# Kernel tuning notes

Hardware: AMD Instinct MI355X
Metric: run time of the kernel (lower is better)

Reference implementation:

```python
import jax, jax.numpy as jnp
import numpy as np

N = 100000
E = 3200000
NEG_SLOPE = 0.2


def _gat(x, W, a_src, a_dst, b, src, dst, n):
    """PyG-style GATConv (eval mode, self-loops already appended to src/dst)."""
    H, C = a_src.shape
    h = (x @ W).reshape(n, H, C)                       # [N,H,C]
    es = jnp.einsum('nhc,hc->nh', h, a_src)            # per-node src logits
    ed = jnp.einsum('nhc,hc->nh', h, a_dst)
    e = jax.nn.leaky_relu(es[src] + ed[dst], NEG_SLOPE)  # [E,H]
    m = jax.ops.segment_max(e, dst, num_segments=n)    # stable softmax per dst
    ee = jnp.exp(e - m[dst])
    z = jax.ops.segment_sum(ee, dst, num_segments=n)
    alpha = ee / z[dst]                                # softmax over in-edges
    out = jax.ops.segment_sum(h[src] * alpha[:, :, None], dst, num_segments=n)
    return out.reshape(n, H * C) + b


def setup_inputs() -> dict:
    key = jax.random.key(0)
    ks = jax.random.split(key, 25)
    rn = lambda k, s, sc=0.1: jax.random.normal(k, s, dtype=jnp.float32) * sc
    return {
        'x1': rn(ks[0], (N, 8), 1.0),
        'x2': rn(ks[1], (N, 10), 1.0),
        'edge_index': jax.random.randint(ks[2], (2, E), 0, N, dtype=jnp.int32),
        'num_nodes': N,
        'Wq': rn(ks[3], (8, 16)), 'bq': rn(ks[4], (16,)),
        'Wk': rn(ks[5], (10, 16)), 'bk': rn(ks[6], (16,)),
        'Wv': rn(ks[7], (18, 16)), 'bv': rn(ks[8], (16,)),
        'W1': rn(ks[9], (16, 32)), 'a1s': rn(ks[10], (8, 4)), 'a1d': rn(ks[11], (8, 4)), 'b1': rn(ks[12], (32,)),
        'W2': rn(ks[13], (32, 16)), 'a2s': rn(ks[14], (4, 4)), 'a2d': rn(ks[15], (4, 4)), 'b2': rn(ks[16], (16,)),
        'W3': rn(ks[17], (16, 8)), 'a3s': rn(ks[18], (2, 4)), 'a3d': rn(ks[19], (2, 4)), 'b3': rn(ks[20], (8,)),
        'Wl2': rn(ks[21], (8, 1)),
    }


def reference(x1, x2, edge_index, num_nodes, Wq, bq, Wk, bk, Wv, bv,
              W1, a1s, a1d, b1, W2, a2s, a2d, b2, W3, a3s, a3d, b3, Wl2):
    n = num_nodes
    q = x1 @ Wq + bq                                   # [N,16]
    k = x2 @ Wk + bk                                   # [N,16]
    v = jnp.concatenate([x1, x2], axis=1) @ Wv + bv    # [N,16]
    score = jnp.sum(q * k, axis=1)                     # bmm(q[:,None,:], k[:,:,None]).squeeze()
    attw = jax.nn.softmax(score)[:, None]              # softmax over all nodes
    fused = attw * v                                   # [N,16]

    sl = jnp.arange(n, dtype=edge_index.dtype)         # GATConv adds self-loops
    src = jnp.concatenate([edge_index[0], sl])
    dst = jnp.concatenate([edge_index[1], sl])

    h1 = _gat(fused, W1, a1s, a1d, b1, src, dst, n)    # [N,32]
    h2 = _gat(h1, W2, a2s, a2d, b2, src, dst, n)       # [N,16]
    x4 = _gat(h2, W3, a3s, a3d, b3, src, dst, n)       # [N,8]; dropout=identity (eval)

    # Row-normalized adjacency (no self loops), expressed as O(E) segment ops.
    r, c = edge_index[0], edge_index[1]
    deg = jax.ops.segment_sum(jnp.ones_like(r, dtype=x4.dtype), r, num_segments=n)
    inv = jnp.where(deg > 0, 1.0 / deg, 0.0)[:, None]
    R3 = jax.ops.segment_sum(x4[c], r, num_segments=n) * inv  # Adj_norm @ x4
    local = jnp.sum(x4 * R3, axis=1, keepdims=True)    # sum_j Adjn[i,j]*(x4_i . x4_j)
    glob = R3 @ Wl2                                    # lin2 (no bias)
    return local + glob                                # [N,1]
```

## Files before the change

kernel.cpp:

```cpp
#include <hip/hip_runtime.h>

#define TPB 256
#define CAP 9216
#define EPB 4096
#define OFSW 784
#define GBPAD 784

typedef float f32x4 __attribute__((ext_vector_type(4)));
typedef float f32x2 __attribute__((ext_vector_type(2)));
typedef unsigned u32x4 __attribute__((ext_vector_type(4)));

__device__ __forceinline__ float lrelu(float x) { return x > 0.f ? x : 0.2f * x; }

__device__ __forceinline__ unsigned bfr(float x) {
  unsigned u = __float_as_uint(x);
  return (u + 0x7FFFu + ((u >> 16) & 1u)) >> 16;
}
__device__ __forceinline__ unsigned pk(float a, float b) { return bfr(a) | (bfr(b) << 16); }
__device__ __forceinline__ float ubf(unsigned us) { return __uint_as_float(us << 16); }

__global__ void __launch_bounds__(TPB) k_bucket(
    const int* __restrict__ ei, int E, int N,
    unsigned* __restrict__ items2, int* __restrict__ ofs)
{
  __shared__ int hist[1024];
  __shared__ int lofs[1024];
  __shared__ int scan_s[TPB];
  __shared__ unsigned stage[2 * EPB];
  int tid = threadIdx.x;
  for (int i = tid; i < 1024; i += TPB) hist[i] = 0;
  int s0 = blockIdx.x * EPB;
  int nE = min(EPB, E - s0);
  int sv[16], dv[16];
  __syncthreads();
#pragma unroll
  for (int k = 0; k < 4; k++) {
    int li = tid * 4 + k * TPB * 4;
    if (li + 3 < nE) {
      int4 s4 = *(const int4*)(ei + s0 + li);
      int4 d4 = *(const int4*)(ei + E + s0 + li);
      sv[k*4+0] = s4.x; sv[k*4+1] = s4.y; sv[k*4+2] = s4.z; sv[k*4+3] = s4.w;
      dv[k*4+0] = d4.x; dv[k*4+1] = d4.y; dv[k*4+2] = d4.z; dv[k*4+3] = d4.w;
#pragma unroll
      for (int j = 0; j < 4; j++) {
        atomicAdd(&hist[dv[k*4+j] >> 8], 1);
        atomicAdd(&hist[(N + sv[k*4+j]) >> 8], 1);
      }
    } else {
      for (int j = 0; j < 4; j++) {
        if (li + j < nE) {
          sv[k*4+j] = ei[s0 + li + j];
          dv[k*4+j] = ei[E + s0 + li + j];
          atomicAdd(&hist[dv[k*4+j] >> 8], 1);
          atomicAdd(&hist[(N + sv[k*4+j]) >> 8], 1);
        }
      }
    }
  }
  __syncthreads();
  int b0 = tid * 4;
  int c0 = hist[b0], c1 = hist[b0 + 1], c2 = hist[b0 + 2], c3 = hist[b0 + 3];
  int tsum = c0 + c1 + c2 + c3;
  scan_s[tid] = tsum;
  __syncthreads();
#pragma unroll
  for (int o = 1; o < TPB; o <<= 1) {
    int t = (tid >= o) ? scan_s[tid - o] : 0;
    __syncthreads();
    scan_s[tid] += t;
    __syncthreads();
  }
  int run = scan_s[tid] - tsum;
  int cs[4] = {c0, c1, c2, c3};
#pragma unroll
  for (int j = 0; j < 4; j++) {
    int b = b0 + j;
    lofs[b] = run;
    hist[b] = 0;
    run += cs[j];
  }
  __syncthreads();
#pragma unroll
  for (int k = 0; k < 16; k++) {
    int li = tid * 4 + (k >> 2) * TPB * 4 + (k & 3);
    if (li < nE) {
      int s = sv[k], d = dv[k];
      int b1 = d >> 8;
      int p1 = lofs[b1] + atomicAdd(&hist[b1], 1);
      stage[p1] = ((unsigned)(d & 255) << 24) | (unsigned)s;
      int k2 = N + s, b2 = k2 >> 8;
      int p2 = lofs[b2] + atomicAdd(&hist[b2], 1);
      stage[p2] = ((unsigned)(k2 & 255) << 24) | (unsigned)d;
    }
  }
  __syncthreads();
  int total = 2 * nE;
  size_t obase = (size_t)blockIdx.x * (2 * EPB);
  for (int idx = tid; idx < total; idx += TPB)
    __builtin_nontemporal_store(stage[idx], items2 + obase + idx);
  int orow = blockIdx.x * OFSW;
  for (int i = tid; i < OFSW; i += TPB)
    ofs[orow + i] = lofs[i];
}

__global__ void __launch_bounds__(TPB) k_t(
    const int* __restrict__ ofs, int* __restrict__ ofsT, int nB)
{
  __shared__ int tile[32][33];
  int lx = threadIdx.x & 31, ly = threadIdx.x >> 5;
  int b0 = blockIdx.y * 32, k0 = blockIdx.x * 32;
#pragma unroll
  for (int r = 0; r < 32; r += 8) {
    int b = b0 + ly + r, k = k0 + lx;
    tile[ly + r][lx] = (b < nB && k < OFSW) ? ofs[b * OFSW + k] : 0;
  }
  __syncthreads();
#pragma unroll
  for (int r = 0; r < 32; r += 8) {
    int k = k0 + ly + r, b = b0 + lx;
    if (k < OFSW && b < GBPAD) ofsT[k * GBPAD + b] = tile[lx][ly + r];
  }
}

__global__ void __launch_bounds__(TPB) k_csr2(
    const int* __restrict__ ofsT, const unsigned* __restrict__ items2, int nB,
    unsigned* __restrict__ items, int* __restrict__ rowptr, int* __restrict__ rowend, int n2)
{
  __shared__ unsigned stage[CAP];
  __shared__ int cnt_s[TPB], scan_s[TPB], off_s[TPB];
  int tid = threadIdx.x, k = blockIdx.x;
  cnt_s[tid] = 0;
  int o0[4], cl[4];
  int tsum = 0;
#pragma unroll
  for (int m = 0; m < 4; m++) {
    int b = tid + m * TPB;
    if (b < nB) {
      int a0 = ofsT[(size_t)k * GBPAD + b];
      int a1 = ofsT[(size_t)(k + 1) * GBPAD + b];
      o0[m] = a0; cl[m] = a1 - a0;
    } else { o0[m] = 0; cl[m] = 0; }
    tsum += cl[m];
  }
  scan_s[tid] = tsum;
  __syncthreads();
#pragma unroll
  for (int o = 1; o < TPB; o <<= 1) {
    int t = (tid >= o) ? scan_s[tid - o] : 0;
    __syncthreads();
    scan_s[tid] += t;
    __syncthreads();
  }
  int cnt = min(scan_s[TPB - 1], CAP);
  int dst = scan_s[tid] - tsum;
#pragma unroll
  for (int m = 0; m < 4; m++) {
    int b = tid + m * TPB;
    const unsigned* src = items2 + (size_t)b * (2 * EPB) + o0[m];
    int c = cl[m];
    int j = 0;
    int head = (4 - (o0[m] & 3)) & 3; if (head > c) head = c;
    for (; j < head; j++) { int p = dst + j; if (p < CAP) stage[p] = src[j]; }
    for (; j + 3 < c; j += 4) {
      u32x4 v = *(const u32x4*)(src + j);
      int p = dst + j;
      if (p + 3 < CAP) {
        stage[p] = v.x; stage[p+1] = v.y; stage[p+2] = v.z; stage[p+3] = v.w;
      } else {
        if (p < CAP) stage[p] = v.x;
        if (p+1 < CAP) stage[p+1] = v.y;
        if (p+2 < CAP) stage[p+2] = v.z;
        if (p+3 < CAP) stage[p+3] = v.w;
      }
    }
    for (; j < c; j++) { int p = dst + j; if (p < CAP) stage[p] = src[j]; }
    dst += c;
  }
  __syncthreads();
  for (int i = tid; i < cnt; i += TPB) atomicAdd(&cnt_s[stage[i] >> 24], 1);
  __syncthreads();
  int v = cnt_s[tid];
  scan_s[tid] = v;
  __syncthreads();
#pragma unroll
  for (int o = 1; o < TPB; o <<= 1) {
    int t = (tid >= o) ? scan_s[tid - o] : 0;
    __syncthreads();
    scan_s[tid] += t;
    __syncthreads();
  }
  int excl = scan_s[tid] - v;
  off_s[tid] = excl;
  size_t bbase = (size_t)k * CAP;
  int g = k * 256 + tid;
  if (g < n2) { rowptr[g] = (int)bbase + excl; rowend[g] = (int)bbase + excl + v; }
  cnt_s[tid] = 0;
  __syncthreads();
  for (int i = tid; i < cnt; i += TPB) {
    unsigned u = stage[i];
    int kk = u >> 24;
    int r = atomicAdd(&cnt_s[kk], 1);
    items[bbase + off_s[kk] + r] = u & 0xFFFFFFu;
  }
}


__global__ void __launch_bounds__(TPB) k_score(
    const float* __restrict__ x1, const float* __restrict__ x2,
    const float* __restrict__ Wq, const float* __restrict__ bq,
    const float* __restrict__ Wk, const float* __restrict__ bk,
    float* __restrict__ escore, float* __restrict__ sumexp, int N)
{
  __shared__ float sWq[128], sWk[160], sbq[16], sbk[16];
  for (int i = threadIdx.x; i < 128; i += TPB) sWq[i] = Wq[i];
  for (int i = threadIdx.x; i < 160; i += TPB) sWk[i] = Wk[i];
  if (threadIdx.x < 16) { sbq[threadIdx.x] = bq[threadIdx.x]; sbk[threadIdx.x] = bk[threadIdx.x]; }
  __syncthreads();
  int n = blockIdx.x * TPB + threadIdx.x;
  float e = 0.f;
  if (n < N) {
    float a[8], b[10];
#pragma unroll
    for (int i = 0; i < 8; i++) a[i] = x1[n*8 + i];
#pragma unroll
    for (int i = 0; i < 10; i++) b[i] = x2[n*10 + i];
    float score = 0.f;
#pragma unroll
    for (int j = 0; j < 16; j++) {
      float q = sbq[j], k = sbk[j];
#pragma unroll
      for (int i = 0; i < 8; i++) q += a[i] * sWq[i*16 + j];
#pragma unroll
      for (int i = 0; i < 10; i++) k += b[i] * sWk[i*16 + j];
      score += q * k;
    }
    e = __expf(score);
    escore[n] = e;
  }
  float v = e;
#pragma unroll
  for (int off = 32; off > 0; off >>= 1) v += __shfl_down(v, off);
  __shared__ float red[TPB / 64];
  if ((threadIdx.x & 63) == 0) red[threadIdx.x >> 6] = v;
  __syncthreads();
  if (threadIdx.x == 0) {
    float s = 0.f;
#pragma unroll
    for (int w = 0; w < TPB / 64; w++) s += red[w];
    atomicAdd(sumexp, s);
  }
}

__global__ void __launch_bounds__(TPB) k_A1(
    const float* __restrict__ x1, const float* __restrict__ x2,
    const float* __restrict__ Wv, const float* __restrict__ bv,
    const float* __restrict__ W1, const float* __restrict__ a1s, const float* __restrict__ a1d,
    const float* __restrict__ escore, const float* __restrict__ sumexp,
    unsigned* __restrict__ rec1a, unsigned* __restrict__ rec1b,
    float* __restrict__ ed, int N)
{
  __shared__ float sWv[288], sbv[16], sW1[512], sas[32], sad[32];
  for (int i = threadIdx.x; i < 288; i += TPB) sWv[i] = Wv[i];
  for (int i = threadIdx.x; i < 512; i += TPB) sW1[i] = W1[i];
  if (threadIdx.x < 16) sbv[threadIdx.x] = bv[threadIdx.x];
  if (threadIdx.x < 32) { sas[threadIdx.x] = a1s[threadIdx.x]; sad[threadIdx.x] = a1d[threadIdx.x]; }
  __syncthreads();
  int n = blockIdx.x * TPB + threadIdx.x;
  if (n >= N) return;
  float w = escore[n] / sumexp[0];
  float f[16];
  {
    float a[8], b[10];
#pragma unroll
    for (int i = 0; i < 8; i++) a[i] = x1[n*8 + i];
#pragma unroll
    for (int i = 0; i < 10; i++) b[i] = x2[n*10 + i];
#pragma unroll
    for (int j = 0; j < 16; j++) {
      float v = sbv[j];
#pragma unroll
      for (int i = 0; i < 8; i++) v += a[i] * sWv[i*16 + j];
#pragma unroll
      for (int i = 0; i < 10; i++) v += b[i] * sWv[(8 + i)*16 + j];
      f[j] = w * v;
    }
  }
  float hr[32], esv[8], edv[8];
#pragma unroll
  for (int j = 0; j < 32; j++) {
    float s = 0.f;
#pragma unroll
    for (int i = 0; i < 16; i++) s += f[i] * sW1[i*32 + j];
    hr[j] = s;
  }
#pragma unroll
  for (int hh = 0; hh < 8; hh++) {
    float s = 0.f, d = 0.f;
#pragma unroll
    for (int c = 0; c < 4; c++) { s += hr[hh*4+c]*sas[hh*4+c]; d += hr[hh*4+c]*sad[hh*4+c]; }
    esv[hh] = s; edv[hh] = d;
  }
  unsigned* ra = rec1a + (size_t)n*10;
  unsigned* rb = rec1b + (size_t)n*10;
  ra[0] = pk(esv[0], esv[1]); ra[1] = pk(esv[2], esv[3]);
  rb[0] = pk(esv[4], esv[5]); rb[1] = pk(esv[6], esv[7]);
#pragma unroll
  for (int hh = 0; hh < 4; hh++) {
    ra[2+2*hh] = pk(hr[hh*4+0], hr[hh*4+1]);
    ra[3+2*hh] = pk(hr[hh*4+2], hr[hh*4+3]);
    rb[2+2*hh] = pk(hr[16+hh*4+0], hr[16+hh*4+1]);
    rb[3+2*hh] = pk(hr[16+hh*4+2], hr[16+hh*4+3]);
  }
  f32x4 e0 = {edv[0], edv[1], edv[2], edv[3]};
  f32x4 e1 = {edv[4], edv[5], edv[6], edv[7]};
  *(f32x4*)(ed + n*8)     = e0;
  *(f32x4*)(ed + n*8 + 4) = e1;
}

__global__ void __launch_bounds__(TPB) k_B2(
    const float* __restrict__ W2, const float* __restrict__ a2s, const float* __restrict__ a2d,
    const float* __restrict__ X,
    unsigned* __restrict__ rec2, float* __restrict__ ed, int N)
{
  __shared__ float sW[512], sas[16], sad[16];
  for (int i = threadIdx.x; i < 512; i += TPB) sW[i] = W2[i];
  if (threadIdx.x < 16) { sas[threadIdx.x] = a2s[threadIdx.x]; sad[threadIdx.x] = a2d[threadIdx.x]; }
  __syncthreads();
  int n = blockIdx.x * TPB + threadIdx.x;
  if (n >= N) return;
  float Xr[32];
#pragma unroll
  for (int i = 0; i < 8; i++) {
    f32x4 t = __builtin_nontemporal_load((const f32x4*)(X + n*32) + i);
    Xr[i*4+0] = t.x; Xr[i*4+1] = t.y; Xr[i*4+2] = t.z; Xr[i*4+3] = t.w;
  }
  float hr[16];
#pragma unroll
  for (int j = 0; j < 16; j++) {
    float s = 0.f;
#pragma unroll
    for (int f = 0; f < 32; f++) s += Xr[f] * sW[f*16 + j];
    hr[j] = s;
  }
  float esv[4], edv[4];
#pragma unroll
  for (int hh = 0; hh < 4; hh++) {
    float s = 0.f, d = 0.f;
#pragma unroll
    for (int c = 0; c < 4; c++) { s += hr[hh*4+c]*sas[hh*4+c]; d += hr[hh*4+c]*sad[hh*4+c]; }
    esv[hh] = s; edv[hh] = d;
  }
  unsigned* r = rec2 + (size_t)n*10;
  r[0] = pk(esv[0], esv[1]); r[1] = pk(esv[2], esv[3]);
#pragma unroll
  for (int hh = 0; hh < 4; hh++) {
    r[2+2*hh] = pk(hr[hh*4+0], hr[hh*4+1]);
    r[3+2*hh] = pk(hr[hh*4+2], hr[hh*4+3]);
  }
  f32x4 e0 = {edv[0], edv[1], edv[2], edv[3]};
  *(f32x4*)(ed + n*8) = e0;
}

__global__ void __launch_bounds__(TPB) k_B3(
    const float* __restrict__ W3, const float* __restrict__ a3s, const float* __restrict__ a3d,
    const float* __restrict__ X3,
    unsigned* __restrict__ rec3, float* __restrict__ ed, int N)
{
  __shared__ float sW[128], sas[8], sad[8];
  for (int i = threadIdx.x; i < 128; i += TPB) sW[i] = W3[i];
  if (threadIdx.x < 8) { sas[threadIdx.x] = a3s[threadIdx.x]; sad[threadIdx.x] = a3d[threadIdx.x]; }
  __syncthreads();
  int n = blockIdx.x * TPB + threadIdx.x;
  if (n >= N) return;
  float Xr[16];
#pragma unroll
  for (int i = 0; i < 4; i++) {
    f32x4 t = __builtin_nontemporal_load((const f32x4*)(X3 + n*16) + i);
    Xr[i*4+0] = t.x; Xr[i*4+1] = t.y; Xr[i*4+2] = t.z; Xr[i*4+3] = t.w;
  }
  float hr[8];
#pragma unroll
  for (int j = 0; j < 8; j++) {
    float s = 0.f;
#pragma unroll
    for (int f = 0; f < 16; f++) s += Xr[f] * sW[f*8 + j];
    hr[j] = s;
  }
  unsigned* r = rec3 + (size_t)n*8;
#pragma unroll
  for (int hh = 0; hh < 2; hh++) {
    float s = 0.f, d = 0.f;
#pragma unroll
    for (int c = 0; c < 4; c++) { s += hr[hh*4+c]*sas[hh*4+c]; d += hr[hh*4+c]*sad[hh*4+c]; }
    u32x4 q = { __float_as_uint(s),
                pk(hr[hh*4+0], hr[hh*4+1]), pk(hr[hh*4+2], hr[hh*4+3]), 0u };
    __builtin_nontemporal_store(q, (u32x4*)(r + hh*4));
    ed[n*8 + hh] = d;
  }
}

template<int OS, int HOFF>
__global__ void __launch_bounds__(TPB) k_gat4(
    const int* __restrict__ rowptr, const int* __restrict__ rowend, const int* __restrict__ col,
    const unsigned* __restrict__ rec, const float* __restrict__ ed,
    const float* __restrict__ bias, float* __restrict__ out, int N)
{
  int wave = (blockIdx.x * TPB + threadIdx.x) >> 6;
  if (wave >= N) return;
  int lane = threadIdx.x & 63;
  int hh = lane & 3, j = lane >> 2;
  int d = wave;
  int e0 = rowptr[d], deg = rowend[d] - e0;
  float edv = ed[d*8 + HOFF + hh];
  float z = 0.f;
  f32x4 acc = {0.f, 0.f, 0.f, 0.f};
  for (int t = j; t <= deg; t += 16) {
    int s = (t == deg) ? d : __builtin_nontemporal_load(col + e0 + t);
    const unsigned* rp = rec + (size_t)s*10;
    unsigned ew = rp[hh >> 1];
    uint2 hv = *(const uint2*)(rp + 2 + 2*hh);
    float esv = ubf((ew >> ((hh & 1) * 16)) & 0xFFFFu);
    float w = __expf(lrelu(esv + edv));
    z += w;
    acc.x += w * ubf(hv.x & 0xFFFFu); acc.y += w * ubf(hv.x >> 16);
    acc.z += w * ubf(hv.y & 0xFFFFu); acc.w += w * ubf(hv.y >> 16);
  }
#pragma unroll
  for (int m = 4; m < 64; m <<= 1) {
    z += __shfl_xor(z, m);
    acc.x += __shfl_xor(acc.x, m); acc.y += __shfl_xor(acc.y, m);
    acc.z += __shfl_xor(acc.z, m); acc.w += __shfl_xor(acc.w, m);
  }
  if (j == 0) {
    float inv = 1.f / z;
    const f32x4 bb = *(const f32x4*)(bias + (HOFF + hh)*4);
    f32x4 o = { acc.x*inv + bb.x, acc.y*inv + bb.y, acc.z*inv + bb.z, acc.w*inv + bb.w };
    __builtin_nontemporal_store(o, (f32x4*)(out + (size_t)d*OS + (HOFF + hh)*4));
  }
}

__global__ void __launch_bounds__(TPB) k_gat3(
    const int* __restrict__ rowptr, const int* __restrict__ rowend, const int* __restrict__ col,
    const unsigned* __restrict__ rec, const float* __restrict__ ed,
    const float* __restrict__ b3, float* __restrict__ x4, int N)
{
  int wave = (blockIdx.x * TPB + threadIdx.x) >> 6;
  if (wave >= N) return;
  int lane = threadIdx.x & 63;
  int hh = lane & 1, j = lane >> 1;
  int d = wave;
  int e0 = rowptr[d], deg = rowend[d] - e0;
  float edv = ed[d*8 + hh];
  float z = 0.f;
  f32x4 acc = {0.f, 0.f, 0.f, 0.f};
  for (int t = j; t <= deg; t += 32) {
    int s = (t == deg) ? d : __builtin_nontemporal_load(col + e0 + t);
    u32x4 q = *(const u32x4*)(rec + (size_t)s*8 + hh*4);
    float w = __expf(lrelu(__uint_as_float(q.x) + edv));
    z += w;
    acc.x += w * ubf(q.y & 0xFFFFu); acc.y += w * ubf(q.y >> 16);
    acc.z += w * ubf(q.z & 0xFFFFu); acc.w += w * ubf(q.z >> 16);
  }
#pragma unroll
  for (int m = 2; m < 64; m <<= 1) {
    z += __shfl_xor(z, m);
    acc.x += __shfl_xor(acc.x, m); acc.y += __shfl_xor(acc.y, m);
    acc.z += __shfl_xor(acc.z, m); acc.w += __shfl_xor(acc.w, m);
  }
  if (j == 0) {
    float inv = 1.f / z;
    const f32x4 bb = *(const f32x4*)(b3 + hh*4);
    f32x4 o = { acc.x*inv + bb.x, acc.y*inv + bb.y, acc.z*inv + bb.z, acc.w*inv + bb.w };
    __builtin_nontemporal_store(o, (f32x4*)(x4 + d*8 + hh*4));
  }
}

__global__ void __launch_bounds__(TPB) k_adj_final(
    const int* __restrict__ rowptr, const int* __restrict__ rowend, const int* __restrict__ col,
    const float* __restrict__ x4, const float* __restrict__ Wl2,
    float* __restrict__ out, int N)
{
  __shared__ float sW[8];
  if (threadIdx.x < 8) sW[threadIdx.x] = Wl2[threadIdx.x];
  __syncthreads();
  int wave = (blockIdx.x * TPB + threadIdx.x) >> 6;
  if (wave >= N) return;
  int lane = threadIdx.x & 63;
  int q = lane & 1, j = lane >> 1;
  int r = wave;
  int e0 = rowptr[N + r], deg = rowend[N + r] - e0;
  f32x4 acc = {0.f, 0.f, 0.f, 0.f};
  for (int t = j; t < deg; t += 32) {
    int c = __builtin_nontemporal_load(col + e0 + t);
    f32x4 xv = *(const f32x4*)(x4 + c*8 + q*4);
    acc.x += xv.x; acc.y += xv.y; acc.z += xv.z; acc.w += xv.w;
  }
#pragma unroll
  for (int m = 2; m < 64; m <<= 1) {
    acc.x += __shfl_xor(acc.x, m); acc.y += __shfl_xor(acc.y, m);
    acc.z += __shfl_xor(acc.z, m); acc.w += __shfl_xor(acc.w, m);
  }
  float part = 0.f;
  if (j == 0) {
    float inv = deg > 0 ? 1.f / (float)deg : 0.f;
    f32x4 R = { acc.x*inv, acc.y*inv, acc.z*inv, acc.w*inv };
    f32x4 xo = *(const f32x4*)(x4 + r*8 + q*4);
    part = xo.x*R.x + xo.y*R.y + xo.z*R.z + xo.w*R.w
         + R.x*sW[q*4+0] + R.y*sW[q*4+1] + R.z*sW[q*4+2] + R.w*sW[q*4+3];
  }
  part += __shfl_xor(part, 1);
  if (lane == 0) out[r] = part;
}

extern "C" void kernel_launch(void* const* d_in, const int* in_sizes, int n_in,
                              void* d_out, int out_size, void* d_ws, size_t ws_size,
                              hipStream_t stream)
{
  const float* x1  = (const float*)d_in[0];
  const float* x2  = (const float*)d_in[1];
  const int*   ei  = (const int*)d_in[2];
  const float* Wq  = (const float*)d_in[4];
  const float* bq  = (const float*)d_in[5];
  const float* Wk  = (const float*)d_in[6];
  const float* bk  = (const float*)d_in[7];
  const float* Wv  = (const float*)d_in[8];
  const float* bv  = (const float*)d_in[9];
  const float* W1  = (const float*)d_in[10];
  const float* a1s = (const float*)d_in[11];
  const float* a1d = (const float*)d_in[12];
  const float* b1  = (const float*)d_in[13];
  const float* W2  = (const float*)d_in[14];
  const float* a2s = (const float*)d_in[15];
  const float* a2d = (const float*)d_in[16];
  const float* b2  = (const float*)d_in[17];
  const float* W3  = (const float*)d_in[18];
  const float* a3s = (const float*)d_in[19];
  const float* a3d = (const float*)d_in[20];
  const float* b3  = (const float*)d_in[21];
  const float* Wl2 = (const float*)d_in[22];

  int N = in_sizes[0] / 8;
  int E = in_sizes[2] / 2;
  int n2 = 2 * N;
  int NB = (n2 + 255) >> 8;
  int gB = (E + EPB - 1) / EPB;

  float* sumexp = (float*)d_ws;
  int* rowptr   = (int*)(sumexp + 16);
  int* rowend   = rowptr + (size_t)n2;
  unsigned* itemsCSR = (unsigned*)(rowend + (size_t)n2);
  unsigned* regionA  = itemsCSR + (size_t)NB * CAP;
  unsigned* items2 = regionA;
  int* ofs  = (int*)(items2 + (size_t)gB * (2 * EPB));
  int* ofsT = ofs + (size_t)gB * OFSW;
  size_t raSize = (size_t)gB * (2 * EPB + OFSW) + (size_t)OFSW * GBPAD;
  unsigned* rec1a = regionA;
  unsigned* rec1b = rec1a + 10ull*N;
  unsigned* rec2  = rec1b + 10ull*N;
  unsigned* rec3  = rec2 + 10ull*N;
  float* ed       = (float*)(rec3 + 8ull*N);
  float* escore   = ed + 8ull*N;
  float* X        = (float*)(regionA + raSize);
  float* X3 = X;
  float* x4 = (float*)rec1b;

  int gN = (N + TPB - 1) / TPB;
  int g64 = (int)(((long long)N * 64 + TPB - 1) / TPB);

  (void)hipMemsetAsync(sumexp, 0, 16 * sizeof(float), stream);

  k_bucket<<<gB, TPB, 0, stream>>>(ei, E, N, items2, ofs);
  dim3 gt((OFSW + 31) / 32, (gB + 31) / 32);
  k_t<<<gt, TPB, 0, stream>>>(ofs, ofsT, gB);
  k_csr2<<<NB, TPB, 0, stream>>>(ofsT, items2, gB, itemsCSR, rowptr, rowend, n2);
  int* colv = (int*)itemsCSR;

  k_score<<<gN, TPB, 0, stream>>>(x1, x2, Wq, bq, Wk, bk, escore, sumexp, N);
  k_A1<<<gN, TPB, 0, stream>>>(x1, x2, Wv, bv, W1, a1s, a1d, escore, sumexp, rec1a, rec1b, ed, N);

  k_gat4<32, 0><<<g64, TPB, 0, stream>>>(rowptr, rowend, colv, rec1a, ed, b1, X, N);
  k_gat4<32, 4><<<g64, TPB, 0, stream>>>(rowptr, rowend, colv, rec1b, ed, b1, X, N);
  k_B2<<<gN, TPB, 0, stream>>>(W2, a2s, a2d, X, rec2, ed, N);
  k_gat4<16, 0><<<g64, TPB, 0, stream>>>(rowptr, rowend, colv, rec2, ed, b2, X3, N);
  k_B3<<<gN, TPB, 0, stream>>>(W3, a3s, a3d, X3, rec3, ed, N);
  k_gat3<<<g64, TPB, 0, stream>>>(rowptr, rowend, colv, rec3, ed, b3, x4, N);

  k_adj_final<<<g64, TPB, 0, stream>>>(rowptr, rowend, colv, x4, Wl2, (float*)d_out, N);
}
```

Baseline: 472.6 us.

## Fuse layer-2 and layer-3 node transforms into GAT aggregation epilogues

Removes the standalone k_B2 and k_B3 kernels. Each node's W2/W3 projection and its attention logits are now computed inside the epilogue of the preceding GAT aggregation wave, using wave shuffles and weights staged in shared memory. Layer-1 output is split so the second-half kernel combines the stored first half with its in-register result, and the third layer's input is never written to memory. This saves two launches and the global round trips of the intermediate features. The cost is extra shuffle and epilogue work in each aggregation wave, plus a shared-memory weight load in every block.

```diff
diff --git a/kernel.cpp b/kernel.cpp
--- a/kernel.cpp
+++ b/kernel.cpp
@@ -317,93 +317,10 @@
   *(f32x4*)(ed + n*8 + 4) = e1;
 }
 
-__global__ void __launch_bounds__(TPB) k_B2(
-    const float* __restrict__ W2, const float* __restrict__ a2s, const float* __restrict__ a2d,
-    const float* __restrict__ X,
-    unsigned* __restrict__ rec2, float* __restrict__ ed, int N)
-{
-  __shared__ float sW[512], sas[16], sad[16];
-  for (int i = threadIdx.x; i < 512; i += TPB) sW[i] = W2[i];
-  if (threadIdx.x < 16) { sas[threadIdx.x] = a2s[threadIdx.x]; sad[threadIdx.x] = a2d[threadIdx.x]; }
-  __syncthreads();
-  int n = blockIdx.x * TPB + threadIdx.x;
-  if (n >= N) return;
-  float Xr[32];
-#pragma unroll
-  for (int i = 0; i < 8; i++) {
-    f32x4 t = __builtin_nontemporal_load((const f32x4*)(X + n*32) + i);
-    Xr[i*4+0] = t.x; Xr[i*4+1] = t.y; Xr[i*4+2] = t.z; Xr[i*4+3] = t.w;
-  }
-  float hr[16];
-#pragma unroll
-  for (int j = 0; j < 16; j++) {
-    float s = 0.f;
-#pragma unroll
-    for (int f = 0; f < 32; f++) s += Xr[f] * sW[f*16 + j];
-    hr[j] = s;
-  }
-  float esv[4], edv[4];
-#pragma unroll
-  for (int hh = 0; hh < 4; hh++) {
-    float s = 0.f, d = 0.f;
-#pragma unroll
-    for (int c = 0; c < 4; c++) { s += hr[hh*4+c]*sas[hh*4+c]; d += hr[hh*4+c]*sad[hh*4+c]; }
-    esv[hh] = s; edv[hh] = d;
-  }
-  unsigned* r = rec2 + (size_t)n*10;
-  r[0] = pk(esv[0], esv[1]); r[1] = pk(esv[2], esv[3]);
-#pragma unroll
-  for (int hh = 0; hh < 4; hh++) {
-    r[2+2*hh] = pk(hr[hh*4+0], hr[hh*4+1]);
-    r[3+2*hh] = pk(hr[hh*4+2], hr[hh*4+3]);
-  }
-  f32x4 e0 = {edv[0], edv[1], edv[2], edv[3]};
-  *(f32x4*)(ed + n*8) = e0;
-}
-
-__global__ void __launch_bounds__(TPB) k_B3(
-    const float* __restrict__ W3, const float* __restrict__ a3s, const float* __restrict__ a3d,
-    const float* __restrict__ X3,
-    unsigned* __restrict__ rec3, float* __restrict__ ed, int N)
-{
-  __shared__ float sW[128], sas[8], sad[8];
-  for (int i = threadIdx.x; i < 128; i += TPB) sW[i] = W3[i];
-  if (threadIdx.x < 8) { sas[threadIdx.x] = a3s[threadIdx.x]; sad[threadIdx.x] = a3d[threadIdx.x]; }
-  __syncthreads();
-  int n = blockIdx.x * TPB + threadIdx.x;
-  if (n >= N) return;
-  float Xr[16];
-#pragma unroll
-  for (int i = 0; i < 4; i++) {
-    f32x4 t = __builtin_nontemporal_load((const f32x4*)(X3 + n*16) + i);
-    Xr[i*4+0] = t.x; Xr[i*4+1] = t.y; Xr[i*4+2] = t.z; Xr[i*4+3] = t.w;
-  }
-  float hr[8];
-#pragma unroll
-  for (int j = 0; j < 8; j++) {
-    float s = 0.f;
-#pragma unroll
-    for (int f = 0; f < 16; f++) s += Xr[f] * sW[f*8 + j];
-    hr[j] = s;
-  }
-  unsigned* r = rec3 + (size_t)n*8;
-#pragma unroll
-  for (int hh = 0; hh < 2; hh++) {
-    float s = 0.f, d = 0.f;
-#pragma unroll
-    for (int c = 0; c < 4; c++) { s += hr[hh*4+c]*sas[hh*4+c]; d += hr[hh*4+c]*sad[hh*4+c]; }
-    u32x4 q = { __float_as_uint(s),
-                pk(hr[hh*4+0], hr[hh*4+1]), pk(hr[hh*4+2], hr[hh*4+3]), 0u };
-    __builtin_nontemporal_store(q, (u32x4*)(r + hh*4));
-    ed[n*8 + hh] = d;
-  }
-}
-
-template<int OS, int HOFF>
-__global__ void __launch_bounds__(TPB) k_gat4(
+__global__ void __launch_bounds__(TPB) k_gat1a(
     const int* __restrict__ rowptr, const int* __restrict__ rowend, const int* __restrict__ col,
     const unsigned* __restrict__ rec, const float* __restrict__ ed,
-    const float* __restrict__ bias, float* __restrict__ out, int N)
+    const float* __restrict__ b1, float* __restrict__ X, int N)
 {
   int wave = (blockIdx.x * TPB + threadIdx.x) >> 6;
   if (wave >= N) return;
@@ -411,7 +328,7 @@
   int hh = lane & 3, j = lane >> 2;
   int d = wave;
   int e0 = rowptr[d], deg = rowend[d] - e0;
-  float edv = ed[d*8 + HOFF + hh];
+  float edv = ed[d*8 + hh];
   float z = 0.f;
   f32x4 acc = {0.f, 0.f, 0.f, 0.f};
   for (int t = j; t <= deg; t += 16) {
@@ -433,10 +350,151 @@
   }
   if (j == 0) {
     float inv = 1.f / z;
-    const f32x4 bb = *(const f32x4*)(bias + (HOFF + hh)*4);
+    const f32x4 bb = *(const f32x4*)(b1 + hh*4);
     f32x4 o = { acc.x*inv + bb.x, acc.y*inv + bb.y, acc.z*inv + bb.z, acc.w*inv + bb.w };
-    __builtin_nontemporal_store(o, (f32x4*)(out + (size_t)d*OS + (HOFF + hh)*4));
-  }
+    __builtin_nontemporal_store(o, (f32x4*)(X + (size_t)d*16 + hh*4));
+  }
+}
+
+__global__ void __launch_bounds__(TPB) k_gat1b(
+    const int* __restrict__ rowptr, const int* __restrict__ rowend, const int* __restrict__ col,
+    const unsigned* __restrict__ rec, const float* __restrict__ ed_rw,
+    const float* __restrict__ b1, const float* __restrict__ X,
+    const float* __restrict__ W2, const float* __restrict__ a2s, const float* __restrict__ a2d,
+    unsigned* __restrict__ rec2, float* __restrict__ edw, int N)
+{
+  __shared__ float sW2[512], sas2[16], sad2[16];
+  for (int i = threadIdx.x; i < 512; i += TPB) sW2[i] = W2[i];
+  if (threadIdx.x < 16) { sas2[threadIdx.x] = a2s[threadIdx.x]; sad2[threadIdx.x] = a2d[threadIdx.x]; }
+  __syncthreads();
+  int wave = (blockIdx.x * TPB + threadIdx.x) >> 6;
+  if (wave >= N) return;
+  int lane = threadIdx.x & 63;
+  int hh = lane & 3, j = lane >> 2;
+  int d = wave;
+  int e0 = rowptr[d], deg = rowend[d] - e0;
+  float edv = ed_rw[d*8 + 4 + hh];
+  float z = 0.f;
+  f32x4 acc = {0.f, 0.f, 0.f, 0.f};
+  for (int t = j; t <= deg; t += 16) {
+    int s = (t == deg) ? d : __builtin_nontemporal_load(col + e0 + t);
+    const unsigned* rp = rec + (size_t)s*10;
+    unsigned ew = rp[hh >> 1];
+    uint2 hv = *(const uint2*)(rp + 2 + 2*hh);
+    float esv = ubf((ew >> ((hh & 1) * 16)) & 0xFFFFu);
+    float w = __expf(lrelu(esv + edv));
+    z += w;
+    acc.x += w * ubf(hv.x & 0xFFFFu); acc.y += w * ubf(hv.x >> 16);
+    acc.z += w * ubf(hv.y & 0xFFFFu); acc.w += w * ubf(hv.y >> 16);
+  }
+#pragma unroll
+  for (int m = 4; m < 64; m <<= 1) {
+    z += __shfl_xor(z, m);
+    acc.x += __shfl_xor(acc.x, m); acc.y += __shfl_xor(acc.y, m);
+    acc.z += __shfl_xor(acc.z, m); acc.w += __shfl_xor(acc.w, m);
+  }
+  float inv = 1.f / z;
+  const f32x4 bb = *(const f32x4*)(b1 + (4 + hh)*4);
+  f32x4 o = { acc.x*inv + bb.x, acc.y*inv + bb.y, acc.z*inv + bb.z, acc.w*inv + bb.w };
+  float xpart = 0.f;
+  if (lane < 16) xpart = X[(size_t)d*16 + lane];
+  float h2 = 0.f;
+#pragma unroll
+  for (int f = 0; f < 16; f++) {
+    float xv = __shfl(xpart, f);
+    if (lane < 16) h2 += xv * sW2[f*16 + lane];
+  }
+#pragma unroll
+  for (int hq = 0; hq < 4; hq++) {
+    float v0 = __shfl(o.x, hq), v1 = __shfl(o.y, hq);
+    float v2 = __shfl(o.z, hq), v3 = __shfl(o.w, hq);
+    if (lane < 16) {
+      h2 += v0 * sW2[(16 + hq*4 + 0)*16 + lane];
+      h2 += v1 * sW2[(16 + hq*4 + 1)*16 + lane];
+      h2 += v2 * sW2[(16 + hq*4 + 2)*16 + lane];
+      h2 += v3 * sW2[(16 + hq*4 + 3)*16 + lane];
+    }
+  }
+  float p_s = 0.f, p_d = 0.f;
+  if (lane < 16) { p_s = h2 * sas2[lane]; p_d = h2 * sad2[lane]; }
+  p_s += __shfl_xor(p_s, 1); p_s += __shfl_xor(p_s, 2);
+  p_d += __shfl_xor(p_d, 1); p_d += __shfl_xor(p_d, 2);
+  unsigned* r2 = rec2 + (size_t)d*10;
+  float ha = __shfl(h2, (lane & 7)*2), hb = __shfl(h2, (lane & 7)*2 + 1);
+  unsigned upk = pk(ha, hb);
+  if (lane < 8) r2[2 + lane] = upk;
+  float es0 = __shfl(p_s, 0), es1 = __shfl(p_s, 4);
+  float es2v = __shfl(p_s, 8), es3v = __shfl(p_s, 12);
+  if (lane == 8) { r2[0] = pk(es0, es1); r2[1] = pk(es2v, es3v); }
+  float edsel = __shfl(p_d, (lane & 3)*4);
+  if (lane < 4) edw[d*8 + lane] = edsel;
+}
+
+__global__ void __launch_bounds__(TPB) k_gat2f(
+    const int* __restrict__ rowptr, const int* __restrict__ rowend, const int* __restrict__ col,
+    const unsigned* __restrict__ rec, const float* __restrict__ ed_rw,
+    const float* __restrict__ b2,
+    const float* __restrict__ W3, const float* __restrict__ a3s, const float* __restrict__ a3d,
+    unsigned* __restrict__ rec3, float* __restrict__ edw, int N)
+{
+  __shared__ float sW3[128], sas3[8], sad3[8];
+  for (int i = threadIdx.x; i < 128; i += TPB) sW3[i] = W3[i];
+  if (threadIdx.x < 8) { sas3[threadIdx.x] = a3s[threadIdx.x]; sad3[threadIdx.x] = a3d[threadIdx.x]; }
+  __syncthreads();
+  int wave = (blockIdx.x * TPB + threadIdx.x) >> 6;
+  if (wave >= N) return;
+  int lane = threadIdx.x & 63;
+  int hh = lane & 3, j = lane >> 2;
+  int d = wave;
+  int e0 = rowptr[d], deg = rowend[d] - e0;
+  float edv = ed_rw[d*8 + hh];
+  float z = 0.f;
+  f32x4 acc = {0.f, 0.f, 0.f, 0.f};
+  for (int t = j; t <= deg; t += 16) {
+    int s = (t == deg) ? d : __builtin_nontemporal_load(col + e0 + t);
+    const unsigned* rp = rec + (size_t)s*10;
+    unsigned ew = rp[hh >> 1];
+    uint2 hv = *(const uint2*)(rp + 2 + 2*hh);
+    float esv = ubf((ew >> ((hh & 1) * 16)) & 0xFFFFu);
+    float w = __expf(lrelu(esv + edv));
+    z += w;
+    acc.x += w * ubf(hv.x & 0xFFFFu); acc.y += w * ubf(hv.x >> 16);
+    acc.z += w * ubf(hv.y & 0xFFFFu); acc.w += w * ubf(hv.y >> 16);
+  }
+#pragma unroll
+  for (int m = 4; m < 64; m <<= 1) {
+    z += __shfl_xor(z, m);
+    acc.x += __shfl_xor(acc.x, m); acc.y += __shfl_xor(acc.y, m);
+    acc.z += __shfl_xor(acc.z, m); acc.w += __shfl_xor(acc.w, m);
+  }
+  float inv = 1.f / z;
+  const f32x4 bb = *(const f32x4*)(b2 + hh*4);
+  f32x4 o = { acc.x*inv + bb.x, acc.y*inv + bb.y, acc.z*inv + bb.z, acc.w*inv + bb.w };
+  float h3 = 0.f;
+#pragma unroll
+  for (int hq = 0; hq < 4; hq++) {
+    float v0 = __shfl(o.x, hq), v1 = __shfl(o.y, hq);
+    float v2 = __shfl(o.z, hq), v3 = __shfl(o.w, hq);
+    if (lane < 8) {
+      h3 += v0 * sW3[(hq*4 + 0)*8 + lane];
+      h3 += v1 * sW3[(hq*4 + 1)*8 + lane];
+      h3 += v2 * sW3[(hq*4 + 2)*8 + lane];
+      h3 += v3 * sW3[(hq*4 + 3)*8 + lane];
+    }
+  }
+  float p_s = 0.f, p_d = 0.f;
+  if (lane < 8) { p_s = h3 * sas3[lane]; p_d = h3 * sad3[lane]; }
+  p_s += __shfl_xor(p_s, 1); p_s += __shfl_xor(p_s, 2);
+  p_d += __shfl_xor(p_d, 1); p_d += __shfl_xor(p_d, 2);
+  float esh = __shfl(p_s, (lane & 1)*4);
+  float h0 = __shfl(h3, (lane & 1)*4 + 0), h1 = __shfl(h3, (lane & 1)*4 + 1);
+  float h2v = __shfl(h3, (lane & 1)*4 + 2), h3v = __shfl(h3, (lane & 1)*4 + 3);
+  if (lane < 2) {
+    u32x4 q = { __float_as_uint(esh), pk(h0, h1), pk(h2v, h3v), 0u };
+    __builtin_nontemporal_store(q, (u32x4*)(rec3 + (size_t)d*8 + lane*4));
+  }
+  float edh = __shfl(p_d, (lane & 1)*4);
+  if (lane < 2) edw[d*8 + lane] = edh;
 }
 
 __global__ void __launch_bounds__(TPB) k_gat3(
@@ -561,7 +619,6 @@
   float* ed       = (float*)(rec3 + 8ull*N);
   float* escore   = ed + 8ull*N;
   float* X        = (float*)(regionA + raSize);
-  float* X3 = X;
   float* x4 = (float*)rec1b;
 
   int gN = (N + TPB - 1) / TPB;
@@ -578,11 +635,11 @@
   k_score<<<gN, TPB, 0, stream>>>(x1, x2, Wq, bq, Wk, bk, escore, sumexp, N);
   k_A1<<<gN, TPB, 0, stream>>>(x1, x2, Wv, bv, W1, a1s, a1d, escore, sumexp, rec1a, rec1b, ed, N);
 
-  k_gat4<32, 0><<<g64, TPB, 0, stream>>>(rowptr, rowend, colv, rec1a, ed, b1, X, N);
-  k_gat4<32, 4><<<g64, TPB, 0, stream>>>(rowptr, rowend, colv, rec1b, ed, b1, X, N);
-  k_B2<<<gN, TPB, 0, stream>>>(W2, a2s, a2d, X, rec2, ed, N);
-  k_gat4<16, 0><<<g64, TPB, 0, stream>>>(rowptr, rowend, colv, rec2, ed, b2, X3, N);
-  k_B3<<<gN, TPB, 0, stream>>>(W3, a3s, a3d, X3, rec3, ed, N);
+  k_gat1a<<<g64, TPB, 0, stream>>>(rowptr, rowend, colv, rec1a, ed, b1, X, N);
+  k_gat1b<<<g64, TPB, 0, stream>>>(rowptr, rowend, colv, rec1b, ed, b1, X,
+                                   W2, a2s, a2d, rec2, ed, N);
+  k_gat2f<<<g64, TPB, 0, stream>>>(rowptr, rowend, colv, rec2, ed, b2,
+                                   W3, a3s, a3d, rec3, ed, N);
   k_gat3<<<g64, TPB, 0, stream>>>(rowptr, rowend, colv, rec3, ed, b3, x4, N);
 
   k_adj_final<<<g64, TPB, 0, stream>>>(rowptr, rowend, colv, x4, Wl2, (float*)d_out, N);
```

Result: slower. 514.3 us (+8.8%).
